# Performance work log

Hardware: AMD Instinct MI355X
Metric: run time of the kernel (lower is better)

Reference implementation:

```python
import jax, jax.numpy as jnp
import numpy as np

NITERS = 5  # mean-field iterations (niters in __init__)


def setup_inputs() -> dict:
    key = jax.random.key(0)
    k1, k2 = jax.random.split(key)
    B, L, C, H, W = 2, 21, 3, 96, 96
    E0 = jax.random.normal(k1, (B, L, H, W), dtype=jnp.float32)
    Refs = jax.random.normal(k2, (B, C, H, W), dtype=jnp.float32)
    # potts_init: weight = ones(L,L) - eye(L)
    Mu_W = jnp.ones((L, L), dtype=jnp.float32) - jnp.eye(L, dtype=jnp.float32)
    return {"E0": E0, "Refs": Refs, "Mu_W": Mu_W}


def _affinity(Refs):
    # Reference-guided dense adjacency (BatchedAdjacency): row-normalized
    # Gaussian affinity on guide features, one N x N matrix per batch element.
    B, C, H, W = Refs.shape
    N = H * W
    f = Refs.reshape(B, C, N).transpose(0, 2, 1)  # [B, N, C]
    sq = jnp.sum(f * f, axis=-1)  # [B, N]
    D = sq[:, :, None] + sq[:, None, :] - 2.0 * jnp.einsum('bnc,bmc->bnm', f, f)
    A = jnp.exp(-0.5 * D)  # [B, N, N]
    return A / jnp.sum(A, axis=-1, keepdims=True)


def reference(E0, Refs, Mu_W):
    B, L, H, W = E0.shape
    N = H * W
    A = _affinity(Refs)  # computed once, reused every iteration
    E0f = E0.reshape(B, L, N)
    Qf = jax.nn.softmax(-E0f, axis=1)  # Q = softmax(-E0, dim=1)
    for _ in range(NITERS):
        # Potts compatibility transform (channel mixing): Mu(Q)
        M = jnp.einsum('kl,bln->bkn', Mu_W, Qf)
        # adjacency message passing: W(Mu(Q), Refs)
        msg = jnp.einsum('bnm,blm->bln', A, M)
        Qf = jax.nn.softmax(-(E0f + msg), axis=1)
    return Qf.reshape(B, L, H, W)
```

## Files before the change

kernel.cpp:

```cpp
#include <hip/hip_runtime.h>
#include <hip/hip_bf16.h>


#define BB 2
#define LL 21
#define LP (LL + 1)
#define NNPX 9216
#define NITERS 5
#define LOG2E 1.4426950408889634f

#define BARRIER() asm volatile("s_waitcnt lgkmcnt(0)\n\ts_barrier" ::: "memory")

typedef __attribute__((ext_vector_type(8))) short short8;
typedef __attribute__((ext_vector_type(4))) float f32x4;
typedef __attribute__((ext_vector_type(4))) unsigned int u32x4;

static __device__ inline unsigned int pk_bf16(float a, float b) {
    __hip_bfloat162 h = __float22bfloat162_rn(make_float2(a, b));
    unsigned int u;
    __builtin_memcpy(&u, &h, 4);
    return u;
}

__global__ __launch_bounds__(256) void k_prep(
        const float* __restrict__ E0, const float* __restrict__ Refs,
        const float* __restrict__ Mu,
        float4* __restrict__ FN, float4* __restrict__ FS,
        __hip_bfloat16* __restrict__ MQ) {
    __shared__ float muS[LL * LL];
    for (int i = threadIdx.x; i < LL * LL; i += 256) muS[i] = Mu[i];
    __syncthreads();

    int idx = blockIdx.x * 256 + threadIdx.x;
    int b = idx / NNPX, n = idx % NNPX;

    const float* rb = Refs + (size_t)b * 3 * NNPX + n;
    float r0 = rb[0], r1 = rb[NNPX], r2 = rb[2 * NNPX];
    FN[idx] = make_float4(r0, r1, r2, 0.f);
    float g = -0.5f * (r0 * r0 + r1 * r1 + r2 * r2);
    FS[idx] = make_float4(g * LOG2E, r0 * LOG2E, r1 * LOG2E, r2 * LOG2E);

    const float* eb = E0 + (size_t)b * LL * NNPX + n;
    float x[LL];
    float mx = -1e30f;
    for (int l = 0; l < LL; ++l) { x[l] = -eb[(size_t)l * NNPX]; mx = fmaxf(mx, x[l]); }
    float s = 0.f;
    for (int l = 0; l < LL; ++l) { x[l] = __builtin_amdgcn_exp2f((x[l] - mx) * LOG2E); s += x[l]; }
    float rs = __builtin_amdgcn_rcpf(s);
    for (int l = 0; l < LL; ++l) x[l] *= rs;

    __hip_bfloat16* mq = MQ + (size_t)b * LL * NNPX + n;
    for (int k = 0; k < LL; ++k) {
        float a = 0.f;
        for (int l = 0; l < LL; ++l) a += muS[k * LL + l] * x[l];
        mq[(size_t)k * NNPX] = __float2bfloat16(a);
    }
}

__global__ __launch_bounds__(256, 4) void k_accum(
        const float4* __restrict__ FS, const float4* __restrict__ FN,
        const unsigned int* __restrict__ MQbf, float* __restrict__ Ppart, int S) {
    __shared__ __align__(16) unsigned short Wlds[2][64 * 72];
    __shared__ __align__(16) unsigned short Mlds[2][21 * 72];

    int t = threadIdx.x;
    int rb = blockIdx.x;
    int s  = blockIdx.y;
    int b  = rb / 144;
    int n0 = (rb % 144) * 64;
    int wv = t >> 6, lane = t & 63;
    int lr = lane & 15, g = lane >> 4;

    int mq = t & 15;
    int ng = t >> 4;
    float4 fnr[4];
    for (int i = 0; i < 4; ++i) fnr[i] = FN[b * NNPX + n0 + ng + 16 * i];

    const int T  = 144 / S;
    const int t0 = s * T;
    const float4* fsb = FS + (size_t)b * NNPX;
    const unsigned int* mqb = MQbf + (size_t)b * LL * (NNPX / 2);

    int sl0 = t >> 5, sm0 = t & 31;
    int sl1 = (t + 256) >> 5, sm1 = (t + 256) & 31;
    int sl2 = (t + 512) >> 5, sm2 = (t + 512) & 31;

    f32x4 acc0 = {0.f, 0.f, 0.f, 0.f};
    f32x4 acc1 = {0.f, 0.f, 0.f, 0.f};

    short8 ones8, zero8;
    {
        u32x4 o = {0x3F803F80u, 0x3F803F80u, 0x3F803F80u, 0x3F803F80u};
        ones8 = __builtin_bit_cast(short8, o);
        u32x4 z = {0u, 0u, 0u, 0u};
        zero8 = __builtin_bit_cast(short8, z);
    }

    float4 fsA0, fsA1, fsA2, fsA3;  unsigned int mrA0, mrA1, mrA2;
    float4 fsB0, fsB1, fsB2, fsB3;  unsigned int mrB0, mrB1, mrB2;

    int row = wv * 16 + lr;

    auto LOADA = [&](int tile) {
        int m0 = (t0 + tile) * 64;
        fsA0 = fsb[m0 + 4 * mq + 0]; fsA1 = fsb[m0 + 4 * mq + 1];
        fsA2 = fsb[m0 + 4 * mq + 2]; fsA3 = fsb[m0 + 4 * mq + 3];
        int mo0 = (t0 + tile) * 32;
        mrA0 = mqb[(size_t)sl0 * (NNPX / 2) + mo0 + sm0];
        mrA1 = mqb[(size_t)sl1 * (NNPX / 2) + mo0 + sm1];
        if (t < 160) mrA2 = mqb[(size_t)sl2 * (NNPX / 2) + mo0 + sm2];
    };
    auto LOADB = [&](int tile) {
        int m0 = (t0 + tile) * 64;
        fsB0 = fsb[m0 + 4 * mq + 0]; fsB1 = fsb[m0 + 4 * mq + 1];
        fsB2 = fsb[m0 + 4 * mq + 2]; fsB3 = fsb[m0 + 4 * mq + 3];
        int mo0 = (t0 + tile) * 32;
        mrB0 = mqb[(size_t)sl0 * (NNPX / 2) + mo0 + sm0];
        mrB1 = mqb[(size_t)sl1 * (NNPX / 2) + mo0 + sm1];
        if (t < 160) mrB2 = mqb[(size_t)sl2 * (NNPX / 2) + mo0 + sm2];
    };
    auto STORE = [&](int buf, const float4& f0, const float4& f1,
                     const float4& f2, const float4& f3,
                     unsigned int m0r, unsigned int m1r, unsigned int m2r) {
        ((unsigned int*)&Mlds[buf][sl0 * 72])[sm0] = m0r;
        ((unsigned int*)&Mlds[buf][sl1 * 72])[sm1] = m1r;
        if (t < 160) ((unsigned int*)&Mlds[buf][sl2 * 72])[sm2] = m2r;
        #pragma unroll
        for (int i = 0; i < 4; ++i) {
            float4 f = fnr[i];
            float w0 = __builtin_amdgcn_exp2f(f0.x + f.x * f0.y + f.y * f0.z + f.z * f0.w);
            float w1 = __builtin_amdgcn_exp2f(f1.x + f.x * f1.y + f.y * f1.z + f.z * f1.w);
            float w2 = __builtin_amdgcn_exp2f(f2.x + f.x * f2.y + f.y * f2.z + f.z * f2.w);
            float w3 = __builtin_amdgcn_exp2f(f3.x + f.x * f3.y + f.y * f3.z + f.z * f3.w);
            uint2 pk;
            pk.x = pk_bf16(w0, w1);
            pk.y = pk_bf16(w2, w3);
            *(uint2*)&Wlds[buf][(ng + 16 * i) * 72 + 4 * mq] = pk;
        }
    };
    auto MFMA = [&](int buf) {
        short8 a0  = *(const short8*)&Wlds[buf][row * 72 + g * 8];
        short8 a1  = *(const short8*)&Wlds[buf][row * 72 + g * 8 + 32];
        short8 b00 = *(const short8*)&Mlds[buf][lr * 72 + g * 8];
        short8 b01 = *(const short8*)&Mlds[buf][lr * 72 + g * 8 + 32];
        short8 b10, b11;
        if (lr < 5) {
            b10 = *(const short8*)&Mlds[buf][(16 + lr) * 72 + g * 8];
            b11 = *(const short8*)&Mlds[buf][(16 + lr) * 72 + g * 8 + 32];
        } else if (lr == 5) {
            b10 = ones8; b11 = ones8;
        } else {
            b10 = zero8; b11 = zero8;
        }
        acc0 = __builtin_amdgcn_mfma_f32_16x16x32_bf16(a0, b00, acc0, 0, 0, 0);
        acc0 = __builtin_amdgcn_mfma_f32_16x16x32_bf16(a1, b01, acc0, 0, 0, 0);
        acc1 = __builtin_amdgcn_mfma_f32_16x16x32_bf16(a0, b10, acc1, 0, 0, 0);
        acc1 = __builtin_amdgcn_mfma_f32_16x16x32_bf16(a1, b11, acc1, 0, 0, 0);
    };

    LOADA(0);
    STORE(0, fsA0, fsA1, fsA2, fsA3, mrA0, mrA1, mrA2);
    LOADB(1);
    BARRIER();

    for (int tt = 0; tt < T; tt += 2) {
        if (tt + 2 < T) LOADA(tt + 2);
        MFMA(0);
        if (tt + 1 < T) STORE(1, fsB0, fsB1, fsB2, fsB3, mrB0, mrB1, mrB2);
        BARRIER();
        if (tt + 3 < T) LOADB(tt + 3);
        if (tt + 1 < T) MFMA(1);
        if (tt + 2 < T) STORE(0, fsA0, fsA1, fsA2, fsA3, mrA0, mrA1, mrA2);
        BARRIER();
    }

    int col = lane & 15, qr = lane >> 4;
    float* pp = Ppart + ((size_t)(s * BB + b) * LP) * NNPX;
    for (int r = 0; r < 4; ++r) {
        int n = n0 + wv * 16 + qr * 4 + r;
        pp[(size_t)col * NNPX + n] = acc0[r];
        if (col < LP - 16) pp[(size_t)(16 + col) * NNPX + n] = acc1[r];
    }
}

template <bool LAST>
__global__ __launch_bounds__(256) void k_softmax(
        const float* __restrict__ E0, const float* __restrict__ Ppart,
        const float* __restrict__ Mu,
        __hip_bfloat16* __restrict__ MQ, float* __restrict__ Out, int S) {
    __shared__ float muS[LL * LL];
    for (int i = threadIdx.x; i < LL * LL; i += 256) muS[i] = Mu[i];
    __syncthreads();

    int idx = blockIdx.x * 256 + threadIdx.x;
    int b = idx / NNPX, n = idx % NNPX;

    float P[LP];
    for (int l = 0; l < LP; ++l) P[l] = 0.f;
    for (int s = 0; s < S; ++s) {
        const float* pp = Ppart + ((size_t)(s * BB + b) * LP) * NNPX + n;
        for (int l = 0; l < LP; ++l) P[l] += pp[(size_t)l * NNPX];
    }
    float rinv = __builtin_amdgcn_rcpf(P[LL]);

    const float* eb = E0 + (size_t)b * LL * NNPX + n;
    float mx = -1e30f;
    for (int l = 0; l < LL; ++l) {
        P[l] = -(eb[(size_t)l * NNPX] + P[l] * rinv);
        mx = fmaxf(mx, P[l]);
    }
    float ssum = 0.f;
    for (int l = 0; l < LL; ++l) { P[l] = __builtin_amdgcn_exp2f((P[l] - mx) * LOG2E); ssum += P[l]; }
    float rs = __builtin_amdgcn_rcpf(ssum);
    for (int l = 0; l < LL; ++l) P[l] *= rs;

    if (LAST) {
        float* ob = Out + (size_t)b * LL * NNPX + n;
        for (int l = 0; l < LL; ++l) ob[(size_t)l * NNPX] = P[l];
    } else {
        __hip_bfloat16* mq = MQ + (size_t)b * LL * NNPX + n;
        for (int k = 0; k < LL; ++k) {
            float a = 0.f;
            for (int l = 0; l < LL; ++l) a += muS[k * LL + l] * P[l];
            mq[(size_t)k * NNPX] = __float2bfloat16(a);
        }
    }
}

extern "C" void kernel_launch(void* const* d_in, const int* in_sizes, int n_in,
                              void* d_out, int out_size, void* d_ws, size_t ws_size,
                              hipStream_t stream) {
    const float* E0   = (const float*)d_in[0];
    const float* Refs = (const float*)d_in[1];
    const float* Mu   = (const float*)d_in[2];
    float* out = (float*)d_out;

    char* w = (char*)d_ws;
    size_t off = 0;
    auto alloc = [&](size_t bytes) {
        void* p = w + off;
        off += (bytes + 255) & ~(size_t)255;
        return p;
    };
    float4* FN     = (float4*)alloc((size_t)BB * NNPX * sizeof(float4));
    float4* FS     = (float4*)alloc((size_t)BB * NNPX * sizeof(float4));
    __hip_bfloat16* MQbf = (__hip_bfloat16*)alloc((size_t)BB * LL * NNPX * sizeof(__hip_bfloat16));

    size_t per = (size_t)BB * LP * NNPX * sizeof(float);
    size_t avail = ws_size > off ? ws_size - off : 0;
    int Smax = (int)(avail / (per + 256));
    static const int divs[] = {8, 6, 4, 3, 2, 1};
    int S = 1;
    for (int i = 0; i < 6; ++i) if (divs[i] <= Smax) { S = divs[i]; break; }
    float* Ppart = (float*)alloc((size_t)S * per);

    k_prep<<<BB * NNPX / 256, 256, 0, stream>>>(E0, Refs, Mu, FN, FS, MQbf);
    for (int it = 0; it < NITERS; ++it) {
        k_accum<<<dim3(288, S), 256, 0, stream>>>(FS, FN, (const unsigned int*)MQbf, Ppart, S);
        if (it == NITERS - 1)
            k_softmax<true><<<BB * NNPX / 256, 256, 0, stream>>>(E0, Ppart, Mu, MQbf, out, S);
        else
            k_softmax<false><<<BB * NNPX / 256, 256, 0, stream>>>(E0, Ppart, Mu, MQbf, out, S);
    }
}
```

Before: 413.3 us.

## Single-buffer LDS tiles in k_accum and raise occupancy target to 8 blocks

Replaces the double-buffered LDS tiles in k_accum with single buffers and restructures the loop into store/barrier/MFMA phases with extra barriers. It also raises launch_bounds min blocks per CU from 4 to 8. The intent is more resident waves to hide latency, in exchange for losing the overlap of affinity computation with MFMA and adding barriers. The new loop assumes T is even (LOADB(tt+1) runs unguarded), and tighter register limits may cause spills.

```diff
diff --git a/kernel.cpp b/kernel.cpp
--- a/kernel.cpp
+++ b/kernel.cpp
@@ -57,11 +57,11 @@
     }
 }
 
-__global__ __launch_bounds__(256, 4) void k_accum(
+__global__ __launch_bounds__(256, 8) void k_accum(
         const float4* __restrict__ FS, const float4* __restrict__ FN,
         const unsigned int* __restrict__ MQbf, float* __restrict__ Ppart, int S) {
-    __shared__ __align__(16) unsigned short Wlds[2][64 * 72];
-    __shared__ __align__(16) unsigned short Mlds[2][21 * 72];
+    __shared__ __align__(16) unsigned short Wlds[64 * 72];
+    __shared__ __align__(16) unsigned short Mlds[21 * 72];
 
     int t = threadIdx.x;
     int rb = blockIdx.x;
@@ -119,12 +119,12 @@
         mrB1 = mqb[(size_t)sl1 * (NNPX / 2) + mo0 + sm1];
         if (t < 160) mrB2 = mqb[(size_t)sl2 * (NNPX / 2) + mo0 + sm2];
     };
-    auto STORE = [&](int buf, const float4& f0, const float4& f1,
+    auto STORE = [&](const float4& f0, const float4& f1,
                      const float4& f2, const float4& f3,
                      unsigned int m0r, unsigned int m1r, unsigned int m2r) {
-        ((unsigned int*)&Mlds[buf][sl0 * 72])[sm0] = m0r;
-        ((unsigned int*)&Mlds[buf][sl1 * 72])[sm1] = m1r;
-        if (t < 160) ((unsigned int*)&Mlds[buf][sl2 * 72])[sm2] = m2r;
+        ((unsigned int*)&Mlds[sl0 * 72])[sm0] = m0r;
+        ((unsigned int*)&Mlds[sl1 * 72])[sm1] = m1r;
+        if (t < 160) ((unsigned int*)&Mlds[sl2 * 72])[sm2] = m2r;
         #pragma unroll
         for (int i = 0; i < 4; ++i) {
             float4 f = fnr[i];
@@ -135,18 +135,18 @@
             uint2 pk;
             pk.x = pk_bf16(w0, w1);
             pk.y = pk_bf16(w2, w3);
-            *(uint2*)&Wlds[buf][(ng + 16 * i) * 72 + 4 * mq] = pk;
+            *(uint2*)&Wlds[(ng + 16 * i) * 72 + 4 * mq] = pk;
         }
     };
-    auto MFMA = [&](int buf) {
-        short8 a0  = *(const short8*)&Wlds[buf][row * 72 + g * 8];
-        short8 a1  = *(const short8*)&Wlds[buf][row * 72 + g * 8 + 32];
-        short8 b00 = *(const short8*)&Mlds[buf][lr * 72 + g * 8];
-        short8 b01 = *(const short8*)&Mlds[buf][lr * 72 + g * 8 + 32];
+    auto MFMA = [&]() {
+        short8 a0  = *(const short8*)&Wlds[row * 72 + g * 8];
+        short8 a1  = *(const short8*)&Wlds[row * 72 + g * 8 + 32];
+        short8 b00 = *(const short8*)&Mlds[lr * 72 + g * 8];
+        short8 b01 = *(const short8*)&Mlds[lr * 72 + g * 8 + 32];
         short8 b10, b11;
         if (lr < 5) {
-            b10 = *(const short8*)&Mlds[buf][(16 + lr) * 72 + g * 8];
-            b11 = *(const short8*)&Mlds[buf][(16 + lr) * 72 + g * 8 + 32];
+            b10 = *(const short8*)&Mlds[(16 + lr) * 72 + g * 8];
+            b11 = *(const short8*)&Mlds[(16 + lr) * 72 + g * 8 + 32];
         } else if (lr == 5) {
             b10 = ones8; b11 = ones8;
         } else {
@@ -159,19 +159,18 @@
     };
 
     LOADA(0);
-    STORE(0, fsA0, fsA1, fsA2, fsA3, mrA0, mrA1, mrA2);
-    LOADB(1);
-    BARRIER();
 
     for (int tt = 0; tt < T; tt += 2) {
+        BARRIER();
+        LOADB(tt + 1);
+        STORE(fsA0, fsA1, fsA2, fsA3, mrA0, mrA1, mrA2);
+        BARRIER();
+        MFMA();
+        BARRIER();
         if (tt + 2 < T) LOADA(tt + 2);
-        MFMA(0);
-        if (tt + 1 < T) STORE(1, fsB0, fsB1, fsB2, fsB3, mrB0, mrB1, mrB2);
-        BARRIER();
-        if (tt + 3 < T) LOADB(tt + 3);
-        if (tt + 1 < T) MFMA(1);
-        if (tt + 2 < T) STORE(0, fsA0, fsA1, fsA2, fsA3, mrA0, mrA1, mrA2);
-        BARRIER();
+        STORE(fsB0, fsB1, fsB2, fsB3, mrB0, mrB1, mrB2);
+        BARRIER();
+        MFMA();
     }
 
     int col = lane & 15, qr = lane >> 4;
```

Measured after the change: 1.567 ms. 279% more time.
